# Kernel tuning notes

Hardware: AMD Instinct MI355X
Metric: run time of the kernel (lower is better)

## Reference

```python
import jax, jax.numpy as jnp
import numpy as np

DIM = 128
N_NODES = 100000
N_EDGES = 200000
M = 800000  # incidence pairs in each direction
L = 2
N_CLASS = 10


def setup_inputs() -> dict:
    key = jax.random.key(0)
    ks = jax.random.split(key, 8)
    s = 1.0 / np.sqrt(DIM)
    return {
        "node_x": jax.random.normal(ks[0], (N_NODES, DIM), jnp.float32),
        "nodes_map": jax.random.randint(ks[1], (M,), 0, N_NODES, jnp.int32),
        "edge_seg": jnp.sort(jax.random.randint(ks[2], (M,), 0, N_EDGES, jnp.int32)),
        "edges_map": jax.random.randint(ks[3], (M,), 0, N_EDGES, jnp.int32),
        "node_seg": jnp.sort(jax.random.randint(ks[4], (M,), 0, N_NODES, jnp.int32)),
        "num_edges": N_EDGES,
        "W_e": jax.random.normal(ks[5], (L, DIM, DIM), jnp.float32) * s,
        "b_e": jnp.zeros((L, DIM), jnp.float32),
        "g_e": jnp.ones((L, DIM), jnp.float32),
        "be_e": jnp.zeros((L, DIM), jnp.float32),
        "W_n": jax.random.normal(ks[6], (L, DIM, DIM), jnp.float32) * s,
        "b_n": jnp.zeros((L, DIM), jnp.float32),
        "g_n": jnp.ones((L, DIM), jnp.float32),
        "be_n": jnp.zeros((L, DIM), jnp.float32),
        "W_c": jax.random.normal(ks[7], (DIM, N_CLASS), jnp.float32) * s,
        "b_c": jnp.zeros((N_CLASS,), jnp.float32),
    }


def _seg_mean(x, seg, num_segments):
    # global_mean_pool: segment sum / count (count clamped to 1 for empty segments)
    s = jax.ops.segment_sum(x, seg, num_segments=num_segments)
    cnt = jax.ops.segment_sum(jnp.ones((x.shape[0],), x.dtype), seg, num_segments=num_segments)
    return s / jnp.maximum(cnt, 1.0)[:, None]


def _layernorm(x, g, b, eps=1e-5):
    m = jnp.mean(x, axis=-1, keepdims=True)
    v = jnp.mean(jnp.square(x - m), axis=-1, keepdims=True)
    return (x - m) * jax.lax.rsqrt(v + eps) * g + b


def reference(node_x, nodes_map, edge_seg, edges_map, node_seg, num_edges,
              W_e, b_e, g_e, be_e, W_n, b_n, g_n, be_n, W_c, b_c):
    n_nodes = node_x.shape[0]
    x = node_x  # in_drp = Dropout(0.0) is identity
    for i in range(W_e.shape[0]):
        # N2E: gather node feats per (edge, member) pair, mean-pool per hyperedge
        ex = _seg_mean(x[nodes_map], edge_seg, num_edges)          # [E, DIM]
        ex = jax.nn.relu(_layernorm(ex @ W_e[i] + b_e[i], g_e[i], be_e[i]))
        # E2N: gather edge feats per (node, incident-edge) pair, mean-pool per node
        x = _seg_mean(ex[edges_map], node_seg, n_nodes)            # [N, DIM]
        x = jax.nn.relu(_layernorm(x @ W_n[i] + b_n[i], g_n[i], be_n[i]))
    return jax.nn.log_softmax(x @ W_c + b_c, axis=-1)
```

## Files before the change

### kernel.cpp

```cpp
#include <hip/hip_runtime.h>
#include <hip/hip_bf16.h>

#define DIM 128

typedef __bf16 bf16x8 __attribute__((ext_vector_type(8)));
typedef float f32x4 __attribute__((ext_vector_type(4)));

static inline int cdiv(int a, int b) { return (a + b - 1) / b; }
static inline size_t align256(size_t x) { return (x + 255) & ~size_t(255); }

__device__ inline unsigned short f2bf(float f) {
    union { float f; unsigned int u; } v; v.f = f;
    unsigned int r = v.u + 0x7fff + ((v.u >> 16) & 1);
    return (unsigned short)(r >> 16);
}
__device__ inline float bf2f(unsigned short h) {
    union { unsigned int u; float f; } v; v.u = ((unsigned int)h) << 16;
    return v.f;
}

__global__ void seg_offsets_kernel(const int* __restrict__ seg, int m, int nseg,
                                   int* __restrict__ off) {
    int s = blockIdx.x * blockDim.x + threadIdx.x;
    if (s > nseg) return;
    int lo = 0, hi = m;
    while (lo < hi) {
        int mid = (lo + hi) >> 1;
        if (seg[mid] < s) lo = mid + 1; else hi = mid;
    }
    off[s] = lo;
}

__global__ void f32_to_bf16_kernel(const float* __restrict__ in,
                                   unsigned short* __restrict__ out, int n4) {
    int i = blockIdx.x * blockDim.x + threadIdx.x;
    if (i >= n4) return;
    float4 v = ((const float4*)in)[i];
    ushort4 o;
    o.x = f2bf(v.x); o.y = f2bf(v.y); o.z = f2bf(v.z); o.w = f2bf(v.w);
    ((ushort4*)out)[i] = o;
}

__global__ void swizzle_w_kernel(const float* __restrict__ W_e, const float* __restrict__ W_n,
                                 unsigned short* __restrict__ wsw) {
    int gid = blockIdx.x * blockDim.x + threadIdx.x;
    int mi = gid >> 11;
    int e = gid & 2047;
    const float* W = (mi < 2) ? (W_e + (size_t)mi * DIM * DIM)
                              : (W_n + (size_t)(mi - 2) * DIM * DIM);
    int t = e >> 9, n = (e >> 6) & 7, lane = e & 63;
    int q = lane >> 4, c = lane & 15;
    int k0 = t * 32 + q * 8, col = n * 16 + c;
    unsigned short vals[8];
#pragma unroll
    for (int j = 0; j < 8; ++j) vals[j] = f2bf(W[(size_t)(k0 + j) * DIM + col]);
    ushort4* dst = (ushort4*)(wsw + (size_t)gid * 8);
    dst[0] = make_ushort4(vals[0], vals[1], vals[2], vals[3]);
    dst[1] = make_ushort4(vals[4], vals[5], vals[6], vals[7]);
}

__device__ inline void accum8(float* a, uint4 v, float wt) {
    unsigned int u[4] = {v.x, v.y, v.z, v.w};
#pragma unroll
    for (int i = 0; i < 4; ++i) {
        union { unsigned int ui; float f; } lo, hi;
        lo.ui = u[i] << 16;
        hi.ui = u[i] & 0xffff0000u;
        a[2 * i]     = fmaf(wt, lo.f, a[2 * i]);
        a[2 * i + 1] = fmaf(wt, hi.f, a[2 * i + 1]);
    }
}

__global__ __launch_bounds__(256)
void fused_pool_gemm_ln_relu_kernel(const uint4* __restrict__ src,
                                    const int* __restrict__ map,
                                    const int* __restrict__ off,
                                    const unsigned short* __restrict__ Wsw,
                                    const float* __restrict__ b,
                                    const float* __restrict__ g,
                                    const float* __restrict__ be,
                                    unsigned short* __restrict__ Y,
                                    int nseg) {
    __shared__ bf16x8 wlds[2048];
    __shared__ unsigned short alds[64][136];
    int tid = threadIdx.x;
    int w = tid >> 6, lane = tid & 63;
    int q = lane >> 4, c = lane & 15;

    {
        const uint4* gsrc = (const uint4*)Wsw;
        uint4* ldst = (uint4*)wlds;
#pragma unroll
        for (int i = 0; i < 8; ++i) ldst[tid + i * 256] = gsrc[tid + i * 256];
    }

    int blockbase = blockIdx.x * 64;
    int qid = w * 4 + q;

    for (int it = 0; it < 4; ++it) {
        int s_local = it * 16 + qid;
        int sc = min(blockbase + s_local, nseg - 1);
        int beg = off[sc], end = off[sc + 1];
        float a[8] = {0.f, 0.f, 0.f, 0.f, 0.f, 0.f, 0.f, 0.f};
        for (int j = beg; j < end; j += 4) {
            int j1 = min(j + 1, end - 1), j2 = min(j + 2, end - 1), j3 = min(j + 3, end - 1);
            int r0 = map[j], r1 = map[j1], r2 = map[j2], r3 = map[j3];
            uint4 v0 = src[(size_t)r0 * 16 + c];
            uint4 v1 = src[(size_t)r1 * 16 + c];
            uint4 v2 = src[(size_t)r2 * 16 + c];
            uint4 v3 = src[(size_t)r3 * 16 + c];
            accum8(a, v0, 1.f);
            accum8(a, v1, (j + 1 < end) ? 1.f : 0.f);
            accum8(a, v2, (j + 2 < end) ? 1.f : 0.f);
            accum8(a, v3, (j + 3 < end) ? 1.f : 0.f);
        }
        float inv = 1.f / fmaxf((float)(end - beg), 1.f);
        uint4 o;
        o.x = (unsigned int)f2bf(a[0] * inv) | ((unsigned int)f2bf(a[1] * inv) << 16);
        o.y = (unsigned int)f2bf(a[2] * inv) | ((unsigned int)f2bf(a[3] * inv) << 16);
        o.z = (unsigned int)f2bf(a[4] * inv) | ((unsigned int)f2bf(a[5] * inv) << 16);
        o.w = (unsigned int)f2bf(a[6] * inv) | ((unsigned int)f2bf(a[7] * inv) << 16);
        *(uint4*)&alds[s_local][c * 8] = o;
    }

    float gcol[8], becol[8];
    f32x4 acc[8];
#pragma unroll
    for (int n = 0; n < 8; ++n) {
        int col = n * 16 + c;
        float bb = b[col];
        gcol[n] = g[col]; becol[n] = be[col];
        acc[n] = f32x4{bb, bb, bb, bb};
    }

    __syncthreads();

    const bf16x8* ap = (const bf16x8*)&alds[w * 16 + c][q * 8];
    bf16x8 a0 = ap[0], a1 = ap[4], a2 = ap[8], a3 = ap[12];

#pragma unroll
    for (int n = 0; n < 8; ++n) {
        acc[n] = __builtin_amdgcn_mfma_f32_16x16x32_bf16(a0, wlds[(0 * 8 + n) * 64 + lane], acc[n], 0, 0, 0);
        acc[n] = __builtin_amdgcn_mfma_f32_16x16x32_bf16(a1, wlds[(1 * 8 + n) * 64 + lane], acc[n], 0, 0, 0);
        acc[n] = __builtin_amdgcn_mfma_f32_16x16x32_bf16(a2, wlds[(2 * 8 + n) * 64 + lane], acc[n], 0, 0, 0);
        acc[n] = __builtin_amdgcn_mfma_f32_16x16x32_bf16(a3, wlds[(3 * 8 + n) * 64 + lane], acc[n], 0, 0, 0);
    }

    float s1[4], s2[4];
#pragma unroll
    for (int j = 0; j < 4; ++j) {
        float t1 = 0.f, t2 = 0.f;
#pragma unroll
        for (int n = 0; n < 8; ++n) { float v = acc[n][j]; t1 += v; t2 = fmaf(v, v, t2); }
        s1[j] = t1; s2[j] = t2;
    }
#pragma unroll
    for (int o = 1; o < 16; o <<= 1)
#pragma unroll
        for (int j = 0; j < 4; ++j) {
            s1[j] += __shfl_xor(s1[j], o);
            s2[j] += __shfl_xor(s2[j], o);
        }

#pragma unroll
    for (int j = 0; j < 4; ++j) {
        int row = blockbase + w * 16 + q * 4 + j;
        if (row >= nseg) continue;
        float m = s1[j] * (1.f / DIM);
        float var = fmaf(-m, m, s2[j] * (1.f / DIM));
        float inv = rsqrtf(var + 1e-5f);
        unsigned short* yp = Y + (size_t)row * DIM + c;
#pragma unroll
        for (int n = 0; n < 8; ++n) {
            float d = acc[n][j] - m;
            float y = fmaxf(fmaf(d * inv, gcol[n], becol[n]), 0.f);
            unsigned int u = __builtin_bit_cast(unsigned int, y) + 0x8000u;
            yp[n * 16] = (unsigned short)(u >> 16);
        }
    }
}

#define CL_ROWS 4
__global__ __launch_bounds__(256)
void classifier_logsoftmax_v3_kernel(const uint4* __restrict__ X,
                                     const float* __restrict__ Wc,
                                     const float* __restrict__ bc,
                                     float* __restrict__ out, int nrows) {
    int w = threadIdx.x >> 6, lane = threadIdx.x & 63;
    int g = lane >> 4, c16 = lane & 15;
    int r0 = (blockIdx.x * 16 + w * 4 + g) * CL_ROWS;
    if (r0 >= nrows) return;

    float wc[8][10];
#pragma unroll
    for (int j = 0; j < 8; ++j)
#pragma unroll
        for (int c = 0; c < 10; ++c) wc[j][c] = Wc[(c16 * 8 + j) * 10 + c];
    float bcv[10];
#pragma unroll
    for (int c = 0; c < 10; ++c) bcv[c] = bc[c];

    int rend = min(r0 + CL_ROWS, nrows);
    for (int r = r0; r < rend; ++r) {
        uint4 v = X[(size_t)r * 16 + c16];
        float x[8];
        {
            unsigned int u[4] = {v.x, v.y, v.z, v.w};
#pragma unroll
            for (int i = 0; i < 4; ++i) {
                union { unsigned int ui; float f; } lo, hi;
                lo.ui = u[i] << 16;
                hi.ui = u[i] & 0xffff0000u;
                x[2 * i] = lo.f; x[2 * i + 1] = hi.f;
            }
        }
        float acc[10];
#pragma unroll
        for (int c = 0; c < 10; ++c) acc[c] = 0.f;
#pragma unroll
        for (int j = 0; j < 8; ++j)
#pragma unroll
            for (int c = 0; c < 10; ++c) acc[c] = fmaf(x[j], wc[j][c], acc[c]);

#pragma unroll
        for (int o = 1; o < 16; o <<= 1)
#pragma unroll
            for (int c = 0; c < 10; ++c) acc[c] += __shfl_xor(acc[c], o);

#pragma unroll
        for (int c = 0; c < 10; ++c) acc[c] += bcv[c];

        float mx = acc[0];
#pragma unroll
        for (int c = 1; c < 10; ++c) mx = fmaxf(mx, acc[c]);
        float se = 0.f;
#pragma unroll
        for (int c = 0; c < 10; ++c) se += expf(acc[c] - mx);
        float lse = mx + logf(se);

        float myv = 0.f;
#pragma unroll
        for (int c = 0; c < 10; ++c) myv = (c16 == c) ? acc[c] : myv;
        if (c16 < 10) out[(size_t)r * 10 + c16] = myv - lse;
    }
}

extern "C" void kernel_launch(void* const* d_in, const int* in_sizes, int n_in,
                              void* d_out, int out_size, void* d_ws, size_t ws_size,
                              hipStream_t stream) {
    const float* node_x    = (const float*)d_in[0];
    const int*   nodes_map = (const int*)d_in[1];
    const int*   edge_seg  = (const int*)d_in[2];
    const int*   edges_map = (const int*)d_in[3];
    const int*   node_seg  = (const int*)d_in[4];
    const float* W_e = (const float*)d_in[6];
    const float* b_e = (const float*)d_in[7];
    const float* g_e = (const float*)d_in[8];
    const float* be_e= (const float*)d_in[9];
    const float* W_n = (const float*)d_in[10];
    const float* b_n = (const float*)d_in[11];
    const float* g_n = (const float*)d_in[12];
    const float* be_n= (const float*)d_in[13];
    const float* W_c = (const float*)d_in[14];
    const float* b_c = (const float*)d_in[15];
    float* out = (float*)d_out;

    const int N = in_sizes[0] / DIM;
    const int M = in_sizes[1];
    const int E = 200000;
    const int L = in_sizes[6] / (DIM * DIM);

    char* ws = (char*)d_ws;
    int* edge_off = (int*)ws;           ws += align256((size_t)(E + 1) * sizeof(int));
    int* node_off = (int*)ws;           ws += align256((size_t)(N + 1) * sizeof(int));
    unsigned short* wsw = (unsigned short*)ws;      ws += align256((size_t)4 * 2048 * 8 * sizeof(unsigned short));
    unsigned short* node_xb = (unsigned short*)ws;  ws += align256((size_t)N * DIM * sizeof(unsigned short));
    unsigned short* exb = (unsigned short*)ws;      ws += align256((size_t)E * DIM * sizeof(unsigned short));
    unsigned short* xb  = (unsigned short*)ws;      ws += align256((size_t)N * DIM * sizeof(unsigned short));
    (void)ws_size;

    seg_offsets_kernel<<<cdiv(E + 1, 256), 256, 0, stream>>>(edge_seg, M, E, edge_off);
    seg_offsets_kernel<<<cdiv(N + 1, 256), 256, 0, stream>>>(node_seg, M, N, node_off);
    f32_to_bf16_kernel<<<cdiv(N * DIM / 4, 256), 256, 0, stream>>>(node_x, node_xb, N * DIM / 4);
    swizzle_w_kernel<<<32, 256, 0, stream>>>(W_e, W_n, wsw);

    const unsigned short* xcur = node_xb;
    for (int i = 0; i < L; ++i) {
        fused_pool_gemm_ln_relu_kernel<<<cdiv(E, 64), 256, 0, stream>>>(
            (const uint4*)xcur, nodes_map, edge_off, wsw + (size_t)i * 16384,
            b_e + i * DIM, g_e + i * DIM, be_e + i * DIM, exb, E);
        fused_pool_gemm_ln_relu_kernel<<<cdiv(N, 64), 256, 0, stream>>>(
            (const uint4*)exb, edges_map, node_off, wsw + (size_t)(2 + i) * 16384,
            b_n + i * DIM, g_n + i * DIM, be_n + i * DIM, xb, N);
        xcur = xb;
    }

    classifier_logsoftmax_v3_kernel<<<cdiv(N, 16 * CL_ROWS), 256, 0, stream>>>(
        (const uint4*)xcur, W_c, b_c, out, N);
}
```

Baseline: 375.8 us.

## Drop LDS weight staging and block barrier; stream weights from global per wave

The 32KB shared-memory weight tile and the cooperative copy are removed. Each wave now loads its MFMA B-fragments straight from global memory (L2-resident), double-buffered across K steps. Rows are now assigned so each wave pools exactly the 16 rows it later multiplies, which lets the __syncthreads be dropped. Segment offsets are prefetched up front and the bf16 rounding is simplified. This cuts LDS use to raise occupancy and removes block-wide sync, at the cost of redundant global weight reads by every wave.

```diff
diff --git a/kernel.cpp b/kernel.cpp
--- a/kernel.cpp
+++ b/kernel.cpp
@@ -14,9 +14,8 @@
     unsigned int r = v.u + 0x7fff + ((v.u >> 16) & 1);
     return (unsigned short)(r >> 16);
 }
-__device__ inline float bf2f(unsigned short h) {
-    union { unsigned int u; float f; } v; v.u = ((unsigned int)h) << 16;
-    return v.f;
+__device__ inline unsigned int hb(float f) {
+    return (__builtin_bit_cast(unsigned int, f) + 0x8000u) >> 16;
 }
 
 __global__ void seg_offsets_kernel(const int* __restrict__ seg, int m, int nseg,
@@ -59,48 +58,52 @@
     dst[1] = make_ushort4(vals[4], vals[5], vals[6], vals[7]);
 }
 
-__device__ inline void accum8(float* a, uint4 v, float wt) {
+__device__ inline void accum8s(float* a, uint4 v, float wt) {
     unsigned int u[4] = {v.x, v.y, v.z, v.w};
 #pragma unroll
     for (int i = 0; i < 4; ++i) {
-        union { unsigned int ui; float f; } lo, hi;
-        lo.ui = u[i] << 16;
-        hi.ui = u[i] & 0xffff0000u;
-        a[2 * i]     = fmaf(wt, lo.f, a[2 * i]);
-        a[2 * i + 1] = fmaf(wt, hi.f, a[2 * i + 1]);
+        float lo = __builtin_bit_cast(float, u[i] << 16);
+        float hi = __builtin_bit_cast(float, u[i]);
+        a[2 * i]     = fmaf(wt, lo, a[2 * i]);
+        a[2 * i + 1] = fmaf(wt, hi, a[2 * i + 1]);
     }
 }
 
 __global__ __launch_bounds__(256)
-void fused_pool_gemm_ln_relu_kernel(const uint4* __restrict__ src,
-                                    const int* __restrict__ map,
-                                    const int* __restrict__ off,
-                                    const unsigned short* __restrict__ Wsw,
-                                    const float* __restrict__ b,
-                                    const float* __restrict__ g,
-                                    const float* __restrict__ be,
-                                    unsigned short* __restrict__ Y,
-                                    int nseg) {
-    __shared__ bf16x8 wlds[2048];
+void fused_pool_gemm_ln_relu_v3_kernel(const uint4* __restrict__ src,
+                                       const int* __restrict__ map,
+                                       const int* __restrict__ off,
+                                       const unsigned short* __restrict__ Wsw,
+                                       const float* __restrict__ b,
+                                       const float* __restrict__ g,
+                                       const float* __restrict__ be,
+                                       unsigned short* __restrict__ Y,
+                                       int nseg) {
     __shared__ unsigned short alds[64][136];
     int tid = threadIdx.x;
     int w = tid >> 6, lane = tid & 63;
     int q = lane >> 4, c = lane & 15;
-
-    {
-        const uint4* gsrc = (const uint4*)Wsw;
-        uint4* ldst = (uint4*)wlds;
-#pragma unroll
-        for (int i = 0; i < 8; ++i) ldst[tid + i * 256] = gsrc[tid + i * 256];
-    }
-
     int blockbase = blockIdx.x * 64;
-    int qid = w * 4 + q;
-
+    int wavebase = w * 16;
+
+    float bcol[8], gcol[8], becol[8];
+#pragma unroll
+    for (int n = 0; n < 8; ++n) {
+        int col = n * 16 + c;
+        bcol[n] = b[col]; gcol[n] = g[col]; becol[n] = be[col];
+    }
+
+    int begv[4], endv[4];
+#pragma unroll
     for (int it = 0; it < 4; ++it) {
-        int s_local = it * 16 + qid;
-        int sc = min(blockbase + s_local, nseg - 1);
-        int beg = off[sc], end = off[sc + 1];
+        int sc = min(blockbase + wavebase + it * 4 + q, nseg - 1);
+        begv[it] = off[sc];
+        endv[it] = off[sc + 1];
+    }
+
+    for (int it = 0; it < 4; ++it) {
+        int s_local = wavebase + it * 4 + q;
+        int beg = begv[it], end = endv[it];
         float a[8] = {0.f, 0.f, 0.f, 0.f, 0.f, 0.f, 0.f, 0.f};
         for (int j = beg; j < end; j += 4) {
             int j1 = min(j + 1, end - 1), j2 = min(j + 2, end - 1), j3 = min(j + 3, end - 1);
@@ -109,41 +112,42 @@
             uint4 v1 = src[(size_t)r1 * 16 + c];
             uint4 v2 = src[(size_t)r2 * 16 + c];
             uint4 v3 = src[(size_t)r3 * 16 + c];
-            accum8(a, v0, 1.f);
-            accum8(a, v1, (j + 1 < end) ? 1.f : 0.f);
-            accum8(a, v2, (j + 2 < end) ? 1.f : 0.f);
-            accum8(a, v3, (j + 3 < end) ? 1.f : 0.f);
+            accum8s(a, v0, 1.f);
+            accum8s(a, v1, (j + 1 < end) ? 1.f : 0.f);
+            accum8s(a, v2, (j + 2 < end) ? 1.f : 0.f);
+            accum8s(a, v3, (j + 3 < end) ? 1.f : 0.f);
         }
         float inv = 1.f / fmaxf((float)(end - beg), 1.f);
         uint4 o;
-        o.x = (unsigned int)f2bf(a[0] * inv) | ((unsigned int)f2bf(a[1] * inv) << 16);
-        o.y = (unsigned int)f2bf(a[2] * inv) | ((unsigned int)f2bf(a[3] * inv) << 16);
-        o.z = (unsigned int)f2bf(a[4] * inv) | ((unsigned int)f2bf(a[5] * inv) << 16);
-        o.w = (unsigned int)f2bf(a[6] * inv) | ((unsigned int)f2bf(a[7] * inv) << 16);
+        o.x = hb(a[0] * inv) | (hb(a[1] * inv) << 16);
+        o.y = hb(a[2] * inv) | (hb(a[3] * inv) << 16);
+        o.z = hb(a[4] * inv) | (hb(a[5] * inv) << 16);
+        o.w = hb(a[6] * inv) | (hb(a[7] * inv) << 16);
         *(uint4*)&alds[s_local][c * 8] = o;
     }
 
-    float gcol[8], becol[8];
     f32x4 acc[8];
 #pragma unroll
-    for (int n = 0; n < 8; ++n) {
-        int col = n * 16 + c;
-        float bb = b[col];
-        gcol[n] = g[col]; becol[n] = be[col];
-        acc[n] = f32x4{bb, bb, bb, bb};
-    }
-
-    __syncthreads();
-
-    const bf16x8* ap = (const bf16x8*)&alds[w * 16 + c][q * 8];
-    bf16x8 a0 = ap[0], a1 = ap[4], a2 = ap[8], a3 = ap[12];
-
-#pragma unroll
-    for (int n = 0; n < 8; ++n) {
-        acc[n] = __builtin_amdgcn_mfma_f32_16x16x32_bf16(a0, wlds[(0 * 8 + n) * 64 + lane], acc[n], 0, 0, 0);
-        acc[n] = __builtin_amdgcn_mfma_f32_16x16x32_bf16(a1, wlds[(1 * 8 + n) * 64 + lane], acc[n], 0, 0, 0);
-        acc[n] = __builtin_amdgcn_mfma_f32_16x16x32_bf16(a2, wlds[(2 * 8 + n) * 64 + lane], acc[n], 0, 0, 0);
-        acc[n] = __builtin_amdgcn_mfma_f32_16x16x32_bf16(a3, wlds[(3 * 8 + n) * 64 + lane], acc[n], 0, 0, 0);
+    for (int n = 0; n < 8; ++n) acc[n] = f32x4{bcol[n], bcol[n], bcol[n], bcol[n]};
+
+    const bf16x8* ap = (const bf16x8*)&alds[wavebase + c][q * 8];
+    bf16x8 afr[4] = {ap[0], ap[4], ap[8], ap[12]};
+
+    const bf16x8* wg = (const bf16x8*)Wsw;
+    bf16x8 wcur[8], wnxt[8];
+#pragma unroll
+    for (int n = 0; n < 8; ++n) wcur[n] = wg[n * 64 + lane];
+#pragma unroll
+    for (int t = 0; t < 4; ++t) {
+        if (t < 3) {
+#pragma unroll
+            for (int n = 0; n < 8; ++n) wnxt[n] = wg[((t + 1) * 8 + n) * 64 + lane];
+        }
+#pragma unroll
+        for (int n = 0; n < 8; ++n)
+            acc[n] = __builtin_amdgcn_mfma_f32_16x16x32_bf16(afr[t], wcur[n], acc[n], 0, 0, 0);
+#pragma unroll
+        for (int n = 0; n < 8; ++n) wcur[n] = wnxt[n];
     }
 
     float s1[4], s2[4];
@@ -164,7 +168,7 @@
 
 #pragma unroll
     for (int j = 0; j < 4; ++j) {
-        int row = blockbase + w * 16 + q * 4 + j;
+        int row = blockbase + wavebase + q * 4 + j;
         if (row >= nseg) continue;
         float m = s1[j] * (1.f / DIM);
         float var = fmaf(-m, m, s2[j] * (1.f / DIM));
@@ -286,10 +290,10 @@
 
     const unsigned short* xcur = node_xb;
     for (int i = 0; i < L; ++i) {
-        fused_pool_gemm_ln_relu_kernel<<<cdiv(E, 64), 256, 0, stream>>>(
+        fused_pool_gemm_ln_relu_v3_kernel<<<cdiv(E, 64), 256, 0, stream>>>(
             (const uint4*)xcur, nodes_map, edge_off, wsw + (size_t)i * 16384,
             b_e + i * DIM, g_e + i * DIM, be_e + i * DIM, exb, E);
-        fused_pool_gemm_ln_relu_kernel<<<cdiv(N, 64), 256, 0, stream>>>(
+        fused_pool_gemm_ln_relu_v3_kernel<<<cdiv(N, 64), 256, 0, stream>>>(
             (const uint4*)exb, edges_map, node_off, wsw + (size_t)(2 + i) * 16384,
             b_n + i * DIM, g_n + i * DIM, be_n + i * DIM, xb, N);
         xcur = xb;
```

After: 365.0 us. 1.03x faster.
